# Performance work log

Hardware: AMD Instinct MI355X
Metric: run time of the kernel (lower is better)

Reference implementation:

```python
import jax, jax.numpy as jnp
import numpy as np

MODEL_DIM = 256
PAIR_IMPORTANCE_WEIGHT = 0.5
B, S, D = 4, 4096, MODEL_DIM


def setup_inputs() -> dict:
    key = jax.random.key(0)
    ks = jax.random.split(key, 6)
    return {
        "query": jax.random.normal(ks[0], (B, S, D), dtype=jnp.float32),
        "key": jax.random.normal(ks[1], (B, S, D), dtype=jnp.float32),
        "value": jax.random.normal(ks[2], (B, S, D), dtype=jnp.float32),
        "W_query": jax.random.normal(ks[3], (D, D), dtype=jnp.float32),
        "W_key": jax.random.normal(ks[4], (D, D), dtype=jnp.float32),
        "W_value": jax.random.normal(ks[5], (D, D), dtype=jnp.float32),
    }


def reference(query, key, value, W_query, W_key, W_value):
    # Projections: [B,S,D] @ [D,D]
    q = jnp.einsum('bsd,de->bse', query, W_query)
    k = jnp.einsum('bsd,de->bse', key, W_key)
    v = jnp.einsum('bsd,de->bse', value, W_value)
    scale = jnp.sqrt(jnp.asarray(MODEL_DIM, dtype=q.dtype))
    # Full [B,S,S] score matrix (global max forces materialization)
    scores = jnp.einsum('bqd,bkd->bqk', q, k) / scale
    s_len = scores.shape[1]
    diag_bias = jnp.eye(s_len, dtype=scores.dtype) * jnp.max(scores)
    scores = scores + PAIR_IMPORTANCE_WEIGHT * diag_bias  # broadcast over batch
    attention_weights = jax.nn.softmax(scores, axis=-1)
    output = jnp.einsum('bqk,bkd->bqd', attention_weights, v)
    return output, attention_weights
```

## Files before the change

### kernel.cpp

```cpp
#include <hip/hip_runtime.h>
#include <cstdint>
#include <cstddef>

#define BB 4
#define SS 4096
#define DD 256
#define SCORE_SCALE (1.0f/16.0f)
#define PIW 0.5f
#define NROWS (BB * SS)

typedef float          f32x4  __attribute__((ext_vector_type(4)));
typedef __bf16         bf16v8 __attribute__((ext_vector_type(8)));
typedef unsigned short u16v8  __attribute__((ext_vector_type(8)));
typedef unsigned short u16v4  __attribute__((ext_vector_type(4)));

__device__ __forceinline__ f32x4 mfma_bf16(u16v8 a, u16v8 b, f32x4 c) {
    return __builtin_amdgcn_mfma_f32_16x16x32_bf16(
        __builtin_bit_cast(bf16v8, a), __builtin_bit_cast(bf16v8, b), c, 0, 0, 0);
}

__device__ __forceinline__ unsigned short f2bf(float f) {
    unsigned u = __float_as_uint(f);
    u += 0x7FFFu + ((u >> 16) & 1u);
    return (unsigned short)(u >> 16);
}
__device__ __forceinline__ float bf2f(unsigned short h) {
    return __uint_as_float(((unsigned)h) << 16);
}
__device__ __forceinline__ unsigned fenc(float x) {
    unsigned u = __float_as_uint(x);
    return (u & 0x80000000u) ? ~u : (u | 0x80000000u);
}
__device__ __forceinline__ float fdec(unsigned e) {
    return __uint_as_float((e & 0x80000000u) ? (e ^ 0x80000000u) : ~e);
}

#define TM 128
#define TN 128
#define TK 16
#define PADW 132

__global__ __launch_bounds__(256) void proj_kernel(
    const float* __restrict__ query, const float* __restrict__ key_, const float* __restrict__ value,
    const float* __restrict__ Wq, const float* __restrict__ Wk, const float* __restrict__ Wv,
    unsigned short* __restrict__ qh, unsigned short* __restrict__ ql,
    unsigned short* __restrict__ kh, unsigned short* __restrict__ kl,
    unsigned short* __restrict__ vT, unsigned* __restrict__ gmax)
{
    const int z = blockIdx.z;
    const float* A = (z == 0) ? query : (z == 1) ? key_ : value;
    const float* W = (z == 0) ? Wq    : (z == 1) ? Wk   : Wv;
    if (z == 0 && blockIdx.x == 0 && blockIdx.y == 0 && threadIdx.x == 0)
        *gmax = 0x007FFFFFu;

    const int K = DD, N = DD;
    __shared__ float As[TK][PADW];
    __shared__ float Bs[TK][PADW];
    const int tid = threadIdx.x;
    const int tx = tid & 15, ty = tid >> 4;
    const int rowBase = blockIdx.y * TM;
    const int colBase = blockIdx.x * TN;

    float acc[8][8] = {};

    for (int k0 = 0; k0 < K; k0 += TK) {
        #pragma unroll
        for (int i = 0; i < 2; i++) {
            int idx = tid + i * 256;
            int r = idx >> 2, kq = idx & 3;
            const float4 av = *(const float4*)&A[(size_t)(rowBase + r) * K + k0 + kq * 4];
            As[kq * 4 + 0][r] = av.x; As[kq * 4 + 1][r] = av.y;
            As[kq * 4 + 2][r] = av.z; As[kq * 4 + 3][r] = av.w;
        }
        #pragma unroll
        for (int i = 0; i < 2; i++) {
            int idx = tid + i * 256;
            int kk = idx >> 5, cq = idx & 31;
            *(float4*)&Bs[kk][cq * 4] = *(const float4*)&W[(size_t)(k0 + kk) * N + colBase + cq * 4];
        }
        __syncthreads();
        #pragma unroll
        for (int kk = 0; kk < TK; kk++) {
            float a[8], b[8];
            *(float4*)&a[0] = *(const float4*)&As[kk][ty * 8];
            *(float4*)&a[4] = *(const float4*)&As[kk][ty * 8 + 4];
            *(float4*)&b[0] = *(const float4*)&Bs[kk][tx * 8];
            *(float4*)&b[4] = *(const float4*)&Bs[kk][tx * 8 + 4];
            #pragma unroll
            for (int i = 0; i < 8; i++)
                #pragma unroll
                for (int j = 0; j < 8; j++)
                    acc[i][j] = fmaf(a[i], b[j], acc[i][j]);
        }
        __syncthreads();
    }

    #pragma unroll
    for (int i = 0; i < 8; i++) {
        const int gr = rowBase + ty * 8 + i;
        if (z == 2) {
            const int b2 = gr >> 12, s2 = gr & (SS - 1);
            #pragma unroll
            for (int j = 0; j < 8; j++) {
                int col = colBase + tx * 8 + j;
                vT[((size_t)b2 * DD + col) * SS + s2] = f2bf(acc[i][j]);
            }
        } else {
            unsigned short h[8], l[8];
            #pragma unroll
            for (int j = 0; j < 8; j++) {
                h[j] = f2bf(acc[i][j]);
                l[j] = f2bf(acc[i][j] - bf2f(h[j]));
            }
            unsigned short* H = (z == 0) ? qh : kh;
            unsigned short* L = (z == 0) ? ql : kl;
            size_t base = (size_t)gr * DD + colBase + tx * 8;
            *(u16v4*)&H[base]     = (u16v4){h[0], h[1], h[2], h[3]};
            *(u16v4*)&H[base + 4] = (u16v4){h[4], h[5], h[6], h[7]};
            *(u16v4*)&L[base]     = (u16v4){l[0], l[1], l[2], l[3]};
            *(u16v4*)&L[base + 4] = (u16v4){l[4], l[5], l[6], l[7]};
        }
    }
}

#define SPAD 40

__global__ __launch_bounds__(256) void scores_mfma(
    const unsigned short* __restrict__ qh, const unsigned short* __restrict__ ql,
    const unsigned short* __restrict__ kh, const unsigned short* __restrict__ kl,
    float* __restrict__ attn, unsigned* __restrict__ gmax,
    float* __restrict__ tmaxg, float* __restrict__ tsumg)
{
    const int b = blockIdx.z;
    const size_t boff = (size_t)b * SS * DD;
    const unsigned short* Qh = qh + boff;
    const unsigned short* Ql = ql + boff;
    const unsigned short* Kh = kh + boff;
    const unsigned short* Kl = kl + boff;
    float* C = attn + (size_t)b * SS * SS;

    __shared__ unsigned short Ah[128][SPAD];
    __shared__ unsigned short Al[128][SPAD];
    __shared__ unsigned short Bh[128][SPAD];
    __shared__ unsigned short Bl[128][SPAD];
    __shared__ float s_m[4][64];
    __shared__ float s_s[4][64];
    __shared__ float red[128];

    const int tid = threadIdx.x;
    const int lane = tid & 63, w = tid >> 6;
    const int wr = (w >> 1) * 64, wc = (w & 1) * 64;
    const int m = lane & 15, qq = lane >> 4;
    const int rowBase = blockIdx.y * 128;
    const int colBase = blockIdx.x * 128;

    f32x4 acc[4][4];
    #pragma unroll
    for (int i = 0; i < 4; i++)
        #pragma unroll
        for (int j = 0; j < 4; j++)
            acc[i][j] = (f32x4){0.f, 0.f, 0.f, 0.f};

    const int chunk = (tid & 3) * 8;
    const int srow  = tid >> 2;

    for (int k0 = 0; k0 < DD; k0 += 32) {
        #pragma unroll
        for (int i = 0; i < 2; i++) {
            int r = srow + i * 64;
            size_t ga = (size_t)(rowBase + r) * DD + k0 + chunk;
            size_t gb = (size_t)(colBase + r) * DD + k0 + chunk;
            *(u16v8*)&Ah[r][chunk] = *(const u16v8*)&Qh[ga];
            *(u16v8*)&Al[r][chunk] = *(const u16v8*)&Ql[ga];
            *(u16v8*)&Bh[r][chunk] = *(const u16v8*)&Kh[gb];
            *(u16v8*)&Bl[r][chunk] = *(const u16v8*)&Kl[gb];
        }
        __syncthreads();

        const int kb = qq * 8;
        u16v8 ah[4], al[4], bh[4], bl[4];
        #pragma unroll
        for (int i = 0; i < 4; i++) {
            ah[i] = *(const u16v8*)&Ah[wr + i * 16 + m][kb];
            al[i] = *(const u16v8*)&Al[wr + i * 16 + m][kb];
            bh[i] = *(const u16v8*)&Bh[wc + i * 16 + m][kb];
            bl[i] = *(const u16v8*)&Bl[wc + i * 16 + m][kb];
        }
        #pragma unroll
        for (int i = 0; i < 4; i++)
            #pragma unroll
            for (int j = 0; j < 4; j++) {
                acc[i][j] = mfma_bf16(ah[i], bh[j], acc[i][j]);
                acc[i][j] = mfma_bf16(ah[i], bl[j], acc[i][j]);
                acc[i][j] = mfma_bf16(al[i], bh[j], acc[i][j]);
            }
        __syncthreads();
    }

    #pragma unroll
    for (int i = 0; i < 4; i++)
        #pragma unroll
        for (int j = 0; j < 4; j++)
            acc[i][j] *= SCORE_SCALE;

    #pragma unroll
    for (int i = 0; i < 4; i++)
        #pragma unroll
        for (int j = 0; j < 4; j++)
            #pragma unroll
            for (int r = 0; r < 4; r++) {
                int row = rowBase + wr + i * 16 + qq * 4 + r;
                int col = colBase + wc + j * 16 + m;
                C[(size_t)row * SS + col] = acc[i][j][r];
            }

    float lmax[16];
    #pragma unroll
    for (int i = 0; i < 4; i++)
        #pragma unroll
        for (int r = 0; r < 4; r++)
            lmax[i * 4 + r] = fmaxf(fmaxf(acc[i][0][r], acc[i][1][r]),
                                    fmaxf(acc[i][2][r], acc[i][3][r]));
    #pragma unroll
    for (int t = 0; t < 16; t++) {
        #pragma unroll
        for (int msk = 1; msk < 16; msk <<= 1)
            lmax[t] = fmaxf(lmax[t], __shfl_xor(lmax[t], msk));
    }
    if (m == 0) {
        #pragma unroll
        for (int i = 0; i < 4; i++)
            #pragma unroll
            for (int r = 0; r < 4; r++)
                s_m[w][i * 16 + qq * 4 + r] = lmax[i * 4 + r];
    }
    __syncthreads();
    float lsum[16];
    #pragma unroll
    for (int i = 0; i < 4; i++)
        #pragma unroll
        for (int r = 0; r < 4; r++) {
            int idx = i * 16 + qq * 4 + r;
            float rm = fmaxf(s_m[w][idx], s_m[w ^ 1][idx]);
            float s = 0.f;
            #pragma unroll
            for (int j = 0; j < 4; j++)
                s += __expf(acc[i][j][r] - rm);
            lsum[i * 4 + r] = s;
        }
    #pragma unroll
    for (int t = 0; t < 16; t++) {
        #pragma unroll
        for (int msk = 1; msk < 16; msk <<= 1)
            lsum[t] += __shfl_xor(lsum[t], msk);
    }
    if (m == 0) {
        #pragma unroll
        for (int i = 0; i < 4; i++)
            #pragma unroll
            for (int r = 0; r < 4; r++)
                s_s[w][i * 16 + qq * 4 + r] = lsum[i * 4 + r];
    }
    __syncthreads();

    if (tid < 128) {
        int wp = tid >> 6, lr = tid & 63;
        float tm = fmaxf(s_m[2 * wp][lr], s_m[2 * wp + 1][lr]);
        float ts = s_s[2 * wp][lr] + s_s[2 * wp + 1][lr];
        size_t gi = (size_t)blockIdx.x * NROWS + (size_t)b * SS + rowBase + tid;
        tmaxg[gi] = tm;
        tsumg[gi] = ts;
        red[tid] = tm;
    }
    __syncthreads();
    for (int s2 = 64; s2 > 0; s2 >>= 1) {
        if (tid < s2) red[tid] = fmaxf(red[tid], red[tid + s2]);
        __syncthreads();
    }
    if (tid == 0) atomicMax(gmax, fenc(red[0]));
}

__global__ __launch_bounds__(256) void stats_merge(
    const float* __restrict__ tmaxg, const float* __restrict__ tsumg,
    const float* __restrict__ attn, const unsigned* __restrict__ gmax,
    float* __restrict__ rowm, float* __restrict__ rowinv)
{
    const int grow = blockIdx.x * 256 + threadIdx.x;
    const int b = grow >> 12, i = grow & (SS - 1);
    const float bias = PIW * fdec(*gmax);

    float tm[32];
    float mx = -INFINITY;
    #pragma unroll
    for (int t = 0; t < 32; t++) {
        tm[t] = tmaxg[(size_t)t * NROWS + grow];
        mx = fmaxf(mx, tm[t]);
    }
    const float dii = attn[(size_t)b * SS * SS + (size_t)i * SS + i];
    mx = fmaxf(mx, dii + bias);

    float s = 0.f;
    #pragma unroll
    for (int t = 0; t < 32; t++)
        s += tsumg[(size_t)t * NROWS + grow] * __expf(tm[t] - mx);
    s += __expf(dii + bias - mx) - __expf(dii - mx);

    rowm[grow] = mx;
    rowinv[grow] = 1.0f / s;
}

#define APAD 72

__global__ __launch_bounds__(256) void av_softmax_mfma(
    float* __restrict__ attn, const unsigned short* __restrict__ vT,
    const float* __restrict__ rowm, const float* __restrict__ rowinv,
    const unsigned* __restrict__ gmax, float* __restrict__ out)
{
    const int b = blockIdx.y;
    const int rowBase = blockIdx.x * 32;
    float* A = attn + (size_t)b * SS * SS;
    const unsigned short* Bv = vT + (size_t)b * DD * SS;
    const float bias = PIW * fdec(*gmax);

    __shared__ unsigned short As[32][APAD];
    __shared__ unsigned short Bs[256][APAD];

    const int tid = threadIdx.x;
    const int lane = tid & 63, w = tid >> 6;
    const int m = lane & 15, qq = lane >> 4;

    const int ch = tid & 15;
    const int ra = tid >> 4;
    float mr[2], ri[2];
    #pragma unroll
    for (int i = 0; i < 2; i++) {
        int rr = rowBase + ra + i * 16;
        mr[i] = rowm[b * SS + rr];
        ri[i] = rowinv[b * SS + rr];
    }

    f32x4 acc[2][4];
    #pragma unroll
    for (int i = 0; i < 2; i++)
        #pragma unroll
        for (int j = 0; j < 4; j++)
            acc[i][j] = (f32x4){0.f, 0.f, 0.f, 0.f};

    for (int k0 = 0; k0 < SS; k0 += 64) {
        #pragma unroll
        for (int i = 0; i < 2; i++) {
            int rr = rowBase + ra + i * 16;
            size_t off = (size_t)rr * SS + k0 + ch * 4;
            float4 t = *(const float4*)&A[off];
            int j0 = k0 + ch * 4;
            float e0 = t.x + ((j0 + 0 == rr) ? bias : 0.0f);
            float e1 = t.y + ((j0 + 1 == rr) ? bias : 0.0f);
            float e2 = t.z + ((j0 + 2 == rr) ? bias : 0.0f);
            float e3 = t.w + ((j0 + 3 == rr) ? bias : 0.0f);
            float w0 = __expf(e0 - mr[i]) * ri[i];
            float w1 = __expf(e1 - mr[i]) * ri[i];
            float w2 = __expf(e2 - mr[i]) * ri[i];
            float w3 = __expf(e3 - mr[i]) * ri[i];
            *(float4*)&A[off] = make_float4(w0, w1, w2, w3);
            *(u16v4*)&As[ra + i * 16][ch * 4] =
                (u16v4){f2bf(w0), f2bf(w1), f2bf(w2), f2bf(w3)};
        }
        {
            const int chb = (tid & 7) * 8;
            #pragma unroll
            for (int i = 0; i < 8; i++) {
                int r = (tid >> 3) + i * 32;
                *(u16v8*)&Bs[r][chb] = *(const u16v8*)&Bv[(size_t)r * SS + k0 + chb];
            }
        }
        __syncthreads();

        #pragma unroll
        for (int kk = 0; kk < 64; kk += 32) {
            const int kb = kk + qq * 8;
            u16v8 af[2], bf[4];
            #pragma unroll
            for (int i = 0; i < 2; i++)
                af[i] = *(const u16v8*)&As[i * 16 + m][kb];
            #pragma unroll
            for (int j = 0; j < 4; j++)
                bf[j] = *(const u16v8*)&Bs[w * 64 + j * 16 + m][kb];
            #pragma unroll
            for (int i = 0; i < 2; i++)
                #pragma unroll
                for (int j = 0; j < 4; j++)
                    acc[i][j] = mfma_bf16(af[i], bf[j], acc[i][j]);
        }
        __syncthreads();
    }

    #pragma unroll
    for (int i = 0; i < 2; i++) {
        #pragma unroll
        for (int j = 0; j < 4; j++) {
            #pragma unroll
            for (int r = 0; r < 4; r++) {
                int row = rowBase + i * 16 + qq * 4 + r;
                int col = w * 64 + j * 16 + m;
                out[((size_t)b * SS + row) * DD + col] = acc[i][j][r];
            }
        }
    }
}

extern "C" void kernel_launch(void* const* d_in, const int* in_sizes, int n_in,
                              void* d_out, int out_size, void* d_ws, size_t ws_size,
                              hipStream_t stream)
{
    const float* query = (const float*)d_in[0];
    const float* key_  = (const float*)d_in[1];
    const float* value = (const float*)d_in[2];
    const float* Wq    = (const float*)d_in[3];
    const float* Wk    = (const float*)d_in[4];
    const float* Wv    = (const float*)d_in[5];

    float* out  = (float*)d_out;
    float* attn = out + (size_t)BB * SS * DD;

    const size_t E = (size_t)BB * SS * DD;
    unsigned short* qh = (unsigned short*)d_ws;
    unsigned short* ql = qh + E;
    unsigned short* kh = ql + E;
    unsigned short* kl = kh + E;
    unsigned short* vT = kl + E;
    float* tmaxg  = (float*)(vT + E);
    float* tsumg  = tmaxg + 32 * (size_t)NROWS;
    float* rowm   = tsumg + 32 * (size_t)NROWS;
    float* rowinv = rowm + NROWS;
    unsigned* gmax = (unsigned*)(rowinv + NROWS);

    proj_kernel<<<dim3(DD / TN, (BB * SS) / TM, 3), 256, 0, stream>>>(
        query, key_, value, Wq, Wk, Wv, qh, ql, kh, kl, vT, gmax);
    scores_mfma<<<dim3(SS / 128, SS / 128, BB), 256, 0, stream>>>(
        qh, ql, kh, kl, attn, gmax, tmaxg, tsumg);
    stats_merge<<<dim3(NROWS / 256), 256, 0, stream>>>(
        tmaxg, tsumg, attn, gmax, rowm, rowinv);
    av_softmax_mfma<<<dim3(SS / 32, BB), 256, 0, stream>>>(
        attn, vT, rowm, rowinv, gmax, out);
}
```

Measured before the change: 729.5 us.

## Pipeline softmax-AV kernel with double-buffered LDS and direct V reads

```diff
diff --git a/kernel.cpp b/kernel.cpp
--- a/kernel.cpp
+++ b/kernel.cpp
@@ -211,7 +211,7 @@
             for (int r = 0; r < 4; r++) {
                 int row = rowBase + wr + i * 16 + qq * 4 + r;
                 int col = colBase + wc + j * 16 + m;
-                C[(size_t)row * SS + col] = acc[i][j][r];
+                __builtin_nontemporal_store(acc[i][j][r], &C[(size_t)row * SS + col]);
             }
 
     float lmax[16];
@@ -309,35 +309,37 @@
     rowinv[grow] = 1.0f / s;
 }
 
-#define APAD 72
-
 __global__ __launch_bounds__(256) void av_softmax_mfma(
     float* __restrict__ attn, const unsigned short* __restrict__ vT,
     const float* __restrict__ rowm, const float* __restrict__ rowinv,
     const unsigned* __restrict__ gmax, float* __restrict__ out)
 {
-    const int b = blockIdx.y;
-    const int rowBase = blockIdx.x * 32;
+    const int lin = blockIdx.x;
+    const int b = (lin & 7) >> 1;
+    const int rowTile = ((lin >> 3) << 1) | (lin & 1);
+    const int rowBase = rowTile * 32;
+
     float* A = attn + (size_t)b * SS * SS;
     const unsigned short* Bv = vT + (size_t)b * DD * SS;
     const float bias = PIW * fdec(*gmax);
 
-    __shared__ unsigned short As[32][APAD];
-    __shared__ unsigned short Bs[256][APAD];
+    __shared__ unsigned short As[2][32][136];
 
     const int tid = threadIdx.x;
     const int lane = tid & 63, w = tid >> 6;
     const int m = lane & 15, qq = lane >> 4;
 
-    const int ch = tid & 15;
-    const int ra = tid >> 4;
-    float mr[2], ri[2];
-    #pragma unroll
-    for (int i = 0; i < 2; i++) {
-        int rr = rowBase + ra + i * 16;
-        mr[i] = rowm[b * SS + rr];
-        ri[i] = rowinv[b * SS + rr];
-    }
+    const int ra = tid >> 3;
+    const int c0 = (tid & 7) * 4;
+    const int rr = rowBase + ra;
+    float* Arow = A + (size_t)rr * SS;
+    const float mr = rowm[b * SS + rr];
+    const float ri = rowinv[b * SS + rr];
+
+    const unsigned short* Bp[4];
+    #pragma unroll
+    for (int j = 0; j < 4; j++)
+        Bp[j] = Bv + (size_t)(w * 64 + j * 16 + m) * SS;
 
     f32x4 acc[2][4];
     #pragma unroll
@@ -346,52 +348,65 @@
         for (int j = 0; j < 4; j++)
             acc[i][j] = (f32x4){0.f, 0.f, 0.f, 0.f};
 
-    for (int k0 = 0; k0 < SS; k0 += 64) {
-        #pragma unroll
-        for (int i = 0; i < 2; i++) {
-            int rr = rowBase + ra + i * 16;
-            size_t off = (size_t)rr * SS + k0 + ch * 4;
-            float4 t = *(const float4*)&A[off];
-            int j0 = k0 + ch * 4;
-            float e0 = t.x + ((j0 + 0 == rr) ? bias : 0.0f);
-            float e1 = t.y + ((j0 + 1 == rr) ? bias : 0.0f);
-            float e2 = t.z + ((j0 + 2 == rr) ? bias : 0.0f);
-            float e3 = t.w + ((j0 + 3 == rr) ? bias : 0.0f);
-            float w0 = __expf(e0 - mr[i]) * ri[i];
-            float w1 = __expf(e1 - mr[i]) * ri[i];
-            float w2 = __expf(e2 - mr[i]) * ri[i];
-            float w3 = __expf(e3 - mr[i]) * ri[i];
-            *(float4*)&A[off] = make_float4(w0, w1, w2, w3);
-            *(u16v4*)&As[ra + i * 16][ch * 4] =
+    f32x4 pf[4];
+
+    auto loadA = [&](int kbase) {
+        #pragma unroll
+        for (int u = 0; u < 4; u++)
+            pf[u] = __builtin_nontemporal_load(
+                (const f32x4*)&Arow[kbase + c0 + u * 32]);
+    };
+    auto procStore = [&](int kbase, int buf) {
+        #pragma unroll
+        for (int u = 0; u < 4; u++) {
+            int c = c0 + u * 32;
+            int j0 = kbase + c;
+            float e0 = pf[u][0] + ((j0 + 0 == rr) ? bias : 0.0f);
+            float e1 = pf[u][1] + ((j0 + 1 == rr) ? bias : 0.0f);
+            float e2 = pf[u][2] + ((j0 + 2 == rr) ? bias : 0.0f);
+            float e3 = pf[u][3] + ((j0 + 3 == rr) ? bias : 0.0f);
+            float w0 = __expf(e0 - mr) * ri;
+            float w1 = __expf(e1 - mr) * ri;
+            float w2 = __expf(e2 - mr) * ri;
+            float w3 = __expf(e3 - mr) * ri;
+            f32x4 wv = (f32x4){w0, w1, w2, w3};
+            __builtin_nontemporal_store(wv, (f32x4*)&Arow[j0]);
+            *(u16v4*)&As[buf][ra][c] =
                 (u16v4){f2bf(w0), f2bf(w1), f2bf(w2), f2bf(w3)};
         }
-        {
-            const int chb = (tid & 7) * 8;
-            #pragma unroll
-            for (int i = 0; i < 8; i++) {
-                int r = (tid >> 3) + i * 32;
-                *(u16v8*)&Bs[r][chb] = *(const u16v8*)&Bv[(size_t)r * SS + k0 + chb];
-            }
-        }
-        __syncthreads();
-
-        #pragma unroll
-        for (int kk = 0; kk < 64; kk += 32) {
-            const int kb = kk + qq * 8;
-            u16v8 af[2], bf[4];
+    };
+
+    const int NT = SS / 128;
+
+    loadA(0);
+    procStore(0, 0);
+    __syncthreads();
+
+    for (int t = 0; t < NT; t++) {
+        const int k0 = t * 128;
+        const int cur = t & 1;
+        if (t + 1 < NT)
+            loadA(k0 + 128);
+        #pragma unroll
+        for (int kk = 0; kk < 4; kk++) {
+            const int kb = kk * 32 + qq * 8;
+            u16v8 bf_[4], af_[2];
+            #pragma unroll
+            for (int j = 0; j < 4; j++)
+                bf_[j] = *(const u16v8*)&Bp[j][k0 + kb];
             #pragma unroll
             for (int i = 0; i < 2; i++)
-                af[i] = *(const u16v8*)&As[i * 16 + m][kb];
-            #pragma unroll
-            for (int j = 0; j < 4; j++)
-                bf[j] = *(const u16v8*)&Bs[w * 64 + j * 16 + m][kb];
+                af_[i] = *(const u16v8*)&As[cur][i * 16 + m][kb];
             #pragma unroll
             for (int i = 0; i < 2; i++)
                 #pragma unroll
                 for (int j = 0; j < 4; j++)
-                    acc[i][j] = mfma_bf16(af[i], bf[j], acc[i][j]);
-        }
-        __syncthreads();
+                    acc[i][j] = mfma_bf16(af_[i], bf_[j], acc[i][j]);
+        }
+        if (t + 1 < NT) {
+            procStore(k0 + 128, cur ^ 1);
+            __syncthreads();
+        }
     }
 
     #pragma unroll
@@ -402,7 +417,8 @@
             for (int r = 0; r < 4; r++) {
                 int row = rowBase + i * 16 + qq * 4 + r;
                 int col = w * 64 + j * 16 + m;
-                out[((size_t)b * SS + row) * DD + col] = acc[i][j][r];
+                __builtin_nontemporal_store(
+                    acc[i][j][r], &out[((size_t)b * SS + row) * DD + col]);
             }
         }
     }
@@ -440,6 +456,6 @@
         qh, ql, kh, kl, attn, gmax, tmaxg, tsumg);
     stats_merge<<<dim3(NROWS / 256), 256, 0, stream>>>(
         tmaxg, tsumg, attn, gmax, rowm, rowinv);
-    av_softmax_mfma<<<dim3(SS / 32, BB), 256, 0, stream>>>(
+    av_softmax_mfma<<<dim3(512), 256, 0, stream>>>(
         attn, vT, rowm, rowinv, gmax, out);
 }
```

New measurement: 672.7 us. 1.08x faster.
